# Kernel tuning notes

Hardware: AMD Instinct MI355X
Metric: run time of the kernel (lower is better)

The kernel has to match this reference:

```python
import jax, jax.numpy as jnp
import numpy as np

D_MODEL = 2048
N_HEADS = 16
N_KV = 4
HEAD_DIM = 128
EPS = 1e-5


def _rmsnorm(x, w, eps=EPS):
    var = jnp.mean(x * x, axis=-1, keepdims=True)
    return x * jax.lax.rsqrt(var + eps) * w


def _rope_cos_sin(seq_len, head_dim, dtype):
    inv_freq = 1.0 / (10000.0 ** (jnp.arange(0, head_dim, 2, dtype=jnp.float32) / head_dim))
    t = jnp.arange(seq_len, dtype=jnp.float32)
    freqs = jnp.outer(t, inv_freq)  # [S, hd/2]
    return jnp.cos(freqs).astype(dtype), jnp.sin(freqs).astype(dtype)


def _apply_rope(x, cos, sin):
    # x: [B,H,S,hd]; cos/sin: [S,hd/2] broadcast as [1,1,S,hd/2]
    half = x.shape[-1] // 2
    x1, x2 = x[..., :half], x[..., half:]
    c = cos[None, None]
    s = sin[None, None]
    return jnp.concatenate([x1 * c - x2 * s, x1 * s + x2 * c], axis=-1)


def setup_inputs() -> dict:
    key = jax.random.key(0)
    ks = jax.random.split(key, 7)
    qkv_out = (N_HEADS + 2 * N_KV) * HEAD_DIM  # 3072
    d = D_MODEL
    inp = {
        "x": jax.random.normal(ks[0], (2, 2048, d), dtype=jnp.float32),
        "w_qkv": jax.random.normal(ks[1], (qkv_out, d), dtype=jnp.float32) * (1.0 / np.sqrt(d)),
        "q_norm_w": jnp.ones((HEAD_DIM,), dtype=jnp.float32),
        "k_norm_w": jnp.ones((HEAD_DIM,), dtype=jnp.float32),
        "w_gate": jax.random.normal(ks[2], (N_HEADS, d), dtype=jnp.float32) * 0.02,
        "b_gate": jnp.ones((N_HEADS,), dtype=jnp.float32),
        "w_o": jax.random.normal(ks[3], (d, N_HEADS * HEAD_DIM), dtype=jnp.float32) * (1.0 / np.sqrt(N_HEADS * HEAD_DIM)),
    }
    return inp


def reference(x, w_qkv, q_norm_w, k_norm_w, w_gate, b_gate, w_o):
    B, S, D = x.shape
    hd = HEAD_DIM
    scale = 1.0 / np.sqrt(hd)
    n_rep = N_HEADS // N_KV

    qkv = jnp.einsum("bsd,od->bso", x, w_qkv)  # [B,S,(H+2KV)*hd]
    q_size = N_HEADS * hd
    kv_size = N_KV * hd
    q = qkv[..., :q_size].reshape(B, S, N_HEADS, hd).transpose(0, 2, 1, 3)
    k = qkv[..., q_size:q_size + kv_size].reshape(B, S, N_KV, hd).transpose(0, 2, 1, 3)
    v = qkv[..., q_size + kv_size:].reshape(B, S, N_KV, hd).transpose(0, 2, 1, 3)

    q = _rmsnorm(q, q_norm_w)
    k = _rmsnorm(k, k_norm_w)

    cos, sin = _rope_cos_sin(S, hd, q.dtype)
    q = _apply_rope(q, cos, sin)
    k = _apply_rope(k, cos, sin)

    # GQA: repeat kv heads
    k = jnp.repeat(k, n_rep, axis=1)  # [B,H,S,hd]
    v = jnp.repeat(v, n_rep, axis=1)

    scores = jnp.einsum("bhqd,bhkd->bhqk", q, k) * scale
    causal = jnp.triu(jnp.ones((S, S), dtype=bool), k=1)
    neg = jnp.finfo(scores.dtype).min
    scores = jnp.where(causal[None, None], neg, scores)
    probs = jax.nn.softmax(scores, axis=-1)
    attn = jnp.einsum("bhqk,bhkd->bhqd", probs, v)  # [B,H,S,hd]

    # g1 gating on attention output per query head
    gate = jax.nn.sigmoid(jnp.einsum("bsd,hd->bsh", x, w_gate) + b_gate)  # [B,S,H]
    attn = attn * gate.transpose(0, 2, 1)[..., None]

    attn = attn.transpose(0, 2, 1, 3).reshape(B, S, N_HEADS * hd)
    out = jnp.einsum("bsf,df->bsd", attn, w_o)
    return out
```

## Files before the change

### kernel.cpp

```cpp
#include <hip/hip_runtime.h>

typedef __bf16 bf16x8 __attribute__((ext_vector_type(8)));
typedef float f32x4 __attribute__((ext_vector_type(4)));

typedef __attribute__((address_space(1))) void gvoid;
typedef __attribute__((address_space(3))) void lvoid;

__device__ __forceinline__ void gl_lds16(const void* g, void* l) {
    __builtin_amdgcn_global_load_lds((gvoid*)g, (lvoid*)l, 16, 0, 0);
}

__device__ __forceinline__ float fin(float v) {
    v = (v == v) ? v : 0.f;
    return fminf(fmaxf(v, -3.0e38f), 3.0e38f);
}

__device__ __forceinline__ bf16x8 cvt8(float4 a, float4 b) {
    bf16x8 r;
    r[0] = (__bf16)a.x; r[1] = (__bf16)a.y; r[2] = (__bf16)a.z; r[3] = (__bf16)a.w;
    r[4] = (__bf16)b.x; r[5] = (__bf16)b.y; r[6] = (__bf16)b.z; r[7] = (__bf16)b.w;
    return r;
}

__device__ __forceinline__ void cvt_range(const float* __restrict__ in,
                                          __bf16* __restrict__ out, int i) {
    const float4* p = (const float4*)in + (size_t)i * 2;
    ((bf16x8*)out)[i] = cvt8(p[0], p[1]);
}

#define SCALE_LOG2E 0.12751666797152713f

__global__ __launch_bounds__(256) void prep_kernel(const float* __restrict__ x,
                                                   const float* __restrict__ wqkv,
                                                   __bf16* __restrict__ xb,
                                                   __bf16* __restrict__ wqb,
                                                   const float* __restrict__ wg,
                                                   const float* __restrict__ bg,
                                                   float* __restrict__ gate,
                                                   float2* __restrict__ ropet) {
    __shared__ float gp[4][16];
    int bid = blockIdx.x, tid = threadIdx.x;
    if (bid < 4096) {
        int lane = tid & 63, wave = tid >> 6;
        const float4* xr = (const float4*)(x + (size_t)bid * 2048);
        float4 p0 = xr[tid * 2], p1 = xr[tid * 2 + 1];
        ((bf16x8*)xb)[bid * 256 + tid] = cvt8(p0, p1);
#pragma unroll
        for (int h = 0; h < 16; ++h) {
            const float4* wr = (const float4*)(wg + (size_t)h * 2048);
            float4 w0 = wr[tid * 2], w1 = wr[tid * 2 + 1];
            float acc = p0.x * w0.x + p0.y * w0.y + p0.z * w0.z + p0.w * w0.w +
                        p1.x * w1.x + p1.y * w1.y + p1.z * w1.z + p1.w * w1.w;
#pragma unroll
            for (int m = 1; m < 64; m <<= 1) acc += __shfl_xor(acc, m);
            if (lane == 0) gp[wave][h] = acc;
        }
        __syncthreads();
        if (tid < 16) {
            int s = bid & 2047, b = bid >> 11;
            float z = gp[0][tid] + gp[1][tid] + gp[2][tid] + gp[3][tid] + bg[tid];
            gate[((size_t)b * 16 + tid) * 2048 + s] = 1.f / (1.f + __expf(-z));
        }
        return;
    }
    if (bid < 7168) {
        cvt_range(wqkv, wqb, (bid - 4096) * 256 + tid);
        return;
    }
    int idx = (bid - 7168) * 256 + tid;
    int s = idx >> 6, d0 = idx & 63;
    float freq = (float)s * __expf(-(float)d0 * (9.2103403719761836f / 64.0f));
    ropet[idx] = make_float2(cosf(freq), sinf(freq));
}

__global__ __launch_bounds__(256) void wo_cvt_kernel(const float* __restrict__ wo,
                                                     __bf16* __restrict__ wob) {
    cvt_range(wo, wob, blockIdx.x * 256 + threadIdx.x);
}

template <int WMT, int WNT, int EPI, typename TC>
__global__ __launch_bounds__(512, 4) void gemm8p(const __bf16* __restrict__ A,
                                                 const __bf16* __restrict__ B,
                                                 TC* __restrict__ C,
                                                 int M, int N, int K, int ldA,
                                                 const float* __restrict__ qw,
                                                 const float* __restrict__ kw,
                                                 const float2* __restrict__ ropet,
                                                 __bf16* __restrict__ Kx) {
    constexpr int BM = WMT * 32;
    constexpr int BN = WNT * 64;
    constexpr int LA = BM / 128;
    constexpr int LB = BN / 128;
    constexpr int VMC = 2 * LA + LB;

    __shared__ __align__(16) __bf16 As[2][BM * 64];
    __shared__ __align__(16) __bf16 Bs[2][BN * 64];

    const int tid = threadIdx.x;
    const int lane = tid & 63, wave = tid >> 6;
    const int wm = wave >> 2, wn = wave & 3;
    const int quad = lane >> 4, mrow = lane & 15;

    const int nbx = gridDim.x;
    const int nwg = nbx * gridDim.y;
    const int orig = (int)blockIdx.y * nbx + (int)blockIdx.x;
    const int wg = (orig & 7) * (nwg >> 3) + (orig >> 3);
    const size_t row0 = (size_t)(wg / nbx) * BM;
    const size_t col0 = (size_t)(wg % nbx) * BN;

    size_t sA[LA], sB[LB];
    int dA[LA], dB[LB];
#pragma unroll
    for (int c = 0; c < LA; ++c) {
        int q = c * 512 + tid;
        int a = q * 16;
        int p = (a >> 4) & 63;
        int rowl = (a >> 11) * 16 + (p >> 2);
        int g = (p & 3) ^ ((p >> 3) & 3);
        int col = ((a >> 10) & 1) * 32 + g * 8;
        sA[c] = (size_t)rowl * ldA + col;
        dA[c] = q * 8;
    }
#pragma unroll
    for (int c = 0; c < LB; ++c) {
        int q = c * 512 + tid;
        int a = q * 16;
        int p = (a >> 4) & 63;
        int rowl = (a >> 11) * 16 + (p >> 2);
        int g = (p & 3) ^ ((p >> 3) & 3);
        int col = ((a >> 10) & 1) * 32 + g * 8;
        sB[c] = (size_t)rowl * K + col;
        dB[c] = q * 8;
    }

    const __bf16* Ag = A + row0 * ldA;
    const __bf16* Bg = B + col0 * K;

    f32x4 acc[WMT][WNT];
#pragma unroll
    for (int i = 0; i < WMT; ++i)
#pragma unroll
        for (int j = 0; j < WNT; ++j) acc[i][j] = (f32x4){0.f, 0.f, 0.f, 0.f};

    const int abase = mrow * 64 + ((quad ^ ((mrow >> 1) & 3)) * 16);

    bf16x8 af[WMT / 2][2], bf[WNT / 2][2];

#define STA8(buf, h, kt)                                                        \
    _Pragma("unroll") for (int c = 0; c < LA; ++c)                              \
        gl_lds16(Ag + (size_t)(h) * (BM / 2) * ldA + (size_t)(kt) * 64 + sA[c], \
                 &As[buf][(h) * (BM / 2) * 64 + dA[c]])

#define STB8(buf, h, kt)                                                        \
    _Pragma("unroll") for (int c = 0; c < LB; ++c)                              \
        gl_lds16(Bg + (size_t)(h) * (BN / 2) * K + (size_t)(kt) * 64 + sB[c],   \
                 &Bs[buf][(h) * (BN / 2) * 64 + dB[c]])

#define LDA8(buf, mh)                                                           \
    _Pragma("unroll") for (int m2 = 0; m2 < WMT / 2; ++m2)                      \
    _Pragma("unroll") for (int s = 0; s < 2; ++s)                               \
        af[m2][s] = *(const bf16x8*)((const char*)&As[buf][0] +                 \
            ((((mh) * (WMT / 2) + m2) * 2 + wm) * 2 + s) * 1024 + abase)

#define LDB8(buf, nh)                                                           \
    _Pragma("unroll") for (int n2 = 0; n2 < WNT / 2; ++n2)                      \
    _Pragma("unroll") for (int s = 0; s < 2; ++s)                               \
        bf[n2][s] = *(const bf16x8*)((const char*)&Bs[buf][0] +                 \
            ((((nh) * (WNT / 2) + n2) * 4 + wn) * 2 + s) * 1024 + abase)

#define MMA8(mh, nh)                                                            \
    _Pragma("unroll") for (int m2 = 0; m2 < WMT / 2; ++m2)                      \
    _Pragma("unroll") for (int n2 = 0; n2 < WNT / 2; ++n2)                      \
    _Pragma("unroll") for (int s = 0; s < 2; ++s)                               \
        acc[(mh) * (WMT / 2) + m2][(nh) * (WNT / 2) + n2] =                     \
            __builtin_amdgcn_mfma_f32_16x16x32_bf16(                            \
                af[m2][s], bf[n2][s],                                           \
                acc[(mh) * (WMT / 2) + m2][(nh) * (WNT / 2) + n2], 0, 0, 0)

#define BAR8 __builtin_amdgcn_s_barrier()

#define WAITVM                                                                  \
    do {                                                                        \
        if constexpr (VMC == 6)                                                 \
            asm volatile("s_waitcnt vmcnt(6)" ::: "memory");                    \
        else if constexpr (VMC == 4)                                            \
            asm volatile("s_waitcnt vmcnt(4)" ::: "memory");                    \
        else                                                                    \
            asm volatile("s_waitcnt vmcnt(3)" ::: "memory");                    \
    } while (0)

#define PHASE_TAIL(mh, nh)                                                      \
    __builtin_amdgcn_s_barrier();                                               \
    asm volatile("s_waitcnt lgkmcnt(0)" ::: "memory");                          \
    __builtin_amdgcn_sched_barrier(0);                                          \
    __builtin_amdgcn_s_setprio(1);                                              \
    MMA8(mh, nh);                                                               \
    __builtin_amdgcn_s_setprio(0)

    const int NT = K / 64;

    STA8(0, 0, 0);
    STB8(0, 0, 0);
    STA8(0, 1, 0);
    STB8(0, 1, 0);
    STA8(1, 0, 1);
    STB8(1, 1, 1);
    STA8(1, 1, 1);
    WAITVM;
    BAR8;

    for (int i = 0; i < NT / 2; ++i) {
        const int u = 2 * i;
        const int k2 = (u + 2 < NT) ? u + 2 : NT - 1;
        const int k3 = (u + 3 < NT) ? u + 3 : NT - 1;
        LDA8(0, 0); LDB8(0, 0); STB8(1, 0, u + 1);
        PHASE_TAIL(0, 0); BAR8;
        LDB8(0, 1); STA8(0, 0, k2);
        PHASE_TAIL(0, 1); BAR8;
        LDA8(0, 1); STB8(0, 1, k2);
        PHASE_TAIL(1, 1); BAR8;
        LDB8(0, 0); STA8(0, 1, k2);
        PHASE_TAIL(1, 0); WAITVM; BAR8;
        LDA8(1, 0); LDB8(1, 0); STB8(0, 0, k2);
        PHASE_TAIL(0, 0); BAR8;
        LDB8(1, 1); STA8(1, 0, k3);
        PHASE_TAIL(0, 1); BAR8;
        LDA8(1, 1); STB8(1, 1, k3);
        PHASE_TAIL(1, 1); BAR8;
        LDB8(1, 0); STA8(1, 1, k3);
        PHASE_TAIL(1, 0); WAITVM; BAR8;
    }
    asm volatile("s_waitcnt vmcnt(0)" ::: "memory");

#undef STA8
#undef STB8
#undef LDA8
#undef LDB8
#undef MMA8
#undef BAR8
#undef WAITVM
#undef PHASE_TAIL

    if constexpr (EPI) {
        int xblk = (int)(col0 >> 7);
        if (xblk < 20) {
            __syncthreads();
            float* sums = (float*)&As[0][0];
            const int d0 = wn * 16 + mrow;
#pragma unroll
            for (int mt = 0; mt < WMT; ++mt) {
                f32x4 p;
#pragma unroll
                for (int r = 0; r < 4; ++r)
                    p[r] = acc[mt][0][r] * acc[mt][0][r] +
                           acc[mt][1][r] * acc[mt][1][r];
#pragma unroll
                for (int m = 1; m < 16; m <<= 1)
#pragma unroll
                    for (int r = 0; r < 4; ++r) p[r] += __shfl_xor(p[r], m);
                if (mrow == 0) {
                    int idx = (((wm * 4 + mt) * 4 + quad) * 4 + wn) * 4;
#pragma unroll
                    for (int r = 0; r < 4; ++r) sums[idx + r] = p[r];
                }
            }
            __syncthreads();
            const bool isQ = (xblk < 16);
            const float* w = isQ ? qw : kw;
            float w1 = w[d0], w2 = w[d0 + 64];
            float osc = isQ ? SCALE_LOG2E : 1.0f;
            int kvh = xblk - 16;
#pragma unroll
            for (int mt = 0; mt < WMT; ++mt) {
                int rbase = (int)row0 + (mt * 2 + wm) * 16 + quad * 4;
                int ib = ((wm * 4 + mt) * 4 + quad) * 16;
                f32x4 sv = *(const f32x4*)&sums[ib] + *(const f32x4*)&sums[ib + 4] +
                           *(const f32x4*)&sums[ib + 8] + *(const f32x4*)&sums[ib + 12];
#pragma unroll
                for (int r = 0; r < 4; ++r) {
                    int row = rbase + r;
                    int s_ = row & 2047, b_ = row >> 11;
                    float inv = rsqrtf(sv[r] * (1.0f / 128.0f) + 1e-5f);
                    float2 cs = ropet[s_ * 64 + d0];
                    float y1 = acc[mt][0][r] * inv * w1;
                    float y2 = acc[mt][1][r] * inv * w2;
                    float v1 = (y1 * cs.x - y2 * cs.y) * osc;
                    float v2 = (y1 * cs.y + y2 * cs.x) * osc;
                    if (isQ) {
                        size_t base = (size_t)row * N + col0 + d0;
                        C[base] = (TC)v1;
                        C[base + 64] = (TC)v2;
                    } else {
                        __bf16* dst = Kx + (((size_t)(b_ * 4 + kvh) * 2048 + s_) << 7);
                        dst[d0] = (__bf16)v1;
                        dst[d0 + 64] = (__bf16)v2;
                    }
                }
            }
            return;
        }
    }

#pragma unroll
    for (int mt = 0; mt < WMT; ++mt)
#pragma unroll
        for (int nt = 0; nt < WNT; ++nt)
#pragma unroll
            for (int r = 0; r < 4; ++r) {
                size_t row = row0 + (mt * 2 + wm) * 16 + quad * 4 + r;
                size_t col = col0 + (nt * 4 + wn) * 16 + mrow;
                C[row * N + col] = (TC)fin(acc[mt][nt][r]);
            }
}

__global__ __launch_bounds__(256) void mid_kernel(const __bf16* __restrict__ qkv,
                                                  __bf16* __restrict__ Vt) {
    __shared__ __align__(16) __bf16 tile[64][72];
    int v = blockIdx.x, t = threadIdx.x;
    int st0 = (v & 31) * 64;
    int dblk = (v >> 5) & 1;
    int bz = v >> 6;
    int b = bz >> 2, kv = bz & 3;
    const __bf16* src = qkv + (size_t)(b * 2048 + st0) * 3072 + 2560 + kv * 128 + dblk * 64;
#pragma unroll
    for (int it = 0; it < 2; ++it) {
        int row = it * 32 + (t >> 3);
        int ch = t & 7;
        *(bf16x8*)&tile[row][ch * 8] = *(const bf16x8*)(src + (size_t)row * 3072 + ch * 8);
    }
    __syncthreads();
    __bf16* dst = Vt + ((size_t)(b * 4 + kv) * 128 + dblk * 64) * 2048 + st0;
#pragma unroll
    for (int it = 0; it < 2; ++it) {
        int drow = it * 32 + (t >> 3);
        int sch = t & 7;
        bf16x8 vv;
#pragma unroll
        for (int j = 0; j < 8; ++j) vv[j] = tile[sch * 8 + j][drow];
        *(bf16x8*)(dst + (size_t)drow * 2048 + sch * 8) = vv;
    }
}

#define FIXED_M 20.0f

#define MFMA16(a, b, c) __builtin_amdgcn_mfma_f32_16x16x32_bf16(a, b, c, 0, 0, 0)

__device__ __forceinline__ int pswz(int e) { return e ^ (((e >> 7) & 1) << 4); }

template <int MODE>
__device__ __forceinline__ void attn_step(const __bf16* Kl, const __bf16* Vl,
                                          int ws, int quad, int mrow,
                                          const bf16x8* aq0, const bf16x8* aq1,
                                          f32x4* o0, f32x4* o1,
                                          f32x4& lf0, f32x4& lf1,
                                          __bf16* Pw) {
    bf16x8 ones;
#pragma unroll
    for (int i = 0; i < 8; ++i) ones[i] = (__bf16)1.0f;

    f32x4 sc0[4], sc1[4];
    __builtin_amdgcn_s_setprio(1);
#pragma unroll
    for (int jt = 0; jt < 4; ++jt) {
        f32x4 s0 = (f32x4){0.f, 0.f, 0.f, 0.f};
        f32x4 s1 = (f32x4){0.f, 0.f, 0.f, 0.f};
#pragma unroll
        for (int dt = 0; dt < 4; ++dt) {
            bf16x8 bk = *(const bf16x8*)&Kl[((dt * 4 + quad) * 64 + jt * 16 + mrow) * 8];
            if (MODE < 2) s0 = MFMA16(aq0[dt], bk, s0);
            s1 = MFMA16(aq1[dt], bk, s1);
        }
        sc0[jt] = s0;
        sc1[jt] = s1;
    }
    __builtin_amdgcn_s_setprio(0);

    if (MODE == 1) {
        int rloc = ws * 16 + quad * 4;
#pragma unroll
        for (int jt = 0; jt < 4; ++jt)
#pragma unroll
            for (int r = 0; r < 4; ++r)
                if (jt * 16 + mrow > rloc + r) sc0[jt][r] = -1e30f;
    }
    if (MODE == 2) {
        int rloc = ws * 16 + quad * 4;
#pragma unroll
        for (int jt = 0; jt < 4; ++jt)
#pragma unroll
            for (int r = 0; r < 4; ++r)
                if (jt * 16 + mrow > rloc + r) sc1[jt][r] = -1e30f;
    }

    const int rb0 = pswz(((0 * 4 + quad) * 16 + mrow) * 8);
    const int rb1 = pswz(((1 * 4 + quad) * 16 + mrow) * 8);
    bf16x8 ap0[2], ap1[2];
    if (MODE < 2) {
#pragma unroll
        for (int jt = 0; jt < 4; ++jt)
#pragma unroll
            for (int r = 0; r < 4; ++r) {
                float pv = exp2f(sc0[jt][r] - FIXED_M);
                int k = jt * 16 + mrow;
                Pw[pswz(((k >> 3) * 16 + quad * 4 + r) * 8 + (k & 7))] = (__bf16)pv;
            }
        ap0[0] = *(const bf16x8*)&Pw[rb0];
        ap0[1] = *(const bf16x8*)&Pw[rb1];
        lf0 = MFMA16(ap0[0], ones, lf0);
        lf0 = MFMA16(ap0[1], ones, lf0);
    }
#pragma unroll
    for (int jt = 0; jt < 4; ++jt)
#pragma unroll
        for (int r = 0; r < 4; ++r) {
            float pv = exp2f(sc1[jt][r] - FIXED_M);
            int k = jt * 16 + mrow;
            Pw[pswz(((k >> 3) * 16 + quad * 4 + r) * 8 + (k & 7))] = (__bf16)pv;
        }
    ap1[0] = *(const bf16x8*)&Pw[rb0];
    ap1[1] = *(const bf16x8*)&Pw[rb1];
    lf1 = MFMA16(ap1[0], ones, lf1);
    lf1 = MFMA16(ap1[1], ones, lf1);

    __builtin_amdgcn_s_setprio(1);
#pragma unroll
    for (int d2 = 0; d2 < 8; ++d2)
#pragma unroll
        for (int ks = 0; ks < 2; ++ks) {
            bf16x8 bv = *(const bf16x8*)&Vl[((ks * 4 + quad) * 128 + d2 * 16 + mrow) * 8];
            if (MODE < 2) o0[d2] = MFMA16(ap0[ks], bv, o0[d2]);
            o1[d2] = MFMA16(ap1[ks], bv, o1[d2]);
        }
    __builtin_amdgcn_s_setprio(0);
}

__global__ __launch_bounds__(512, 2) void attn_kernel(__bf16* __restrict__ qkvO,
                                                      const __bf16* __restrict__ Kx,
                                                      const __bf16* __restrict__ Vt,
                                                      const float* __restrict__ gate) {
    __shared__ __align__(16) __bf16 Kl[2][2][64 * 128];
    __shared__ __align__(16) __bf16 Vl[2][2][128 * 64];
    __shared__ __align__(16) __bf16 Pl[8][1024];
    int tid = threadIdx.x, lane = tid & 63, wave = tid >> 6;

    int ws = wave & 3, st = wave >> 2;
    int quad = lane >> 4, mrow = lane & 15;
    __bf16* Pw = &Pl[wave][0];

    int idx = blockIdx.x;
    int qb = 15 - (idx >> 5);
    int h = idx & 15, b = (idx >> 4) & 1;
    int kvh = h >> 2;

    int sst = tid >> 8, lt = tid & 255;
    const __bf16* kbase = Kx + (size_t)(b * 4 + kvh) * 2048 * 128 + (lt & 63) * 128 + (lt >> 6) * 8;
    const __bf16* vbase = Vt + (size_t)(b * 4 + kvh) * 128 * 2048 + (lt & 127) * 2048 + (lt >> 7) * 8;
    int ldst = lt * 8;

    auto STAGE = [&](int buf, int tile) {
        const __bf16* kp = kbase + (size_t)tile * 8192;
        const __bf16* vp = vbase + (size_t)tile * 64;
#pragma unroll
        for (int c = 0; c < 4; ++c) gl_lds16(kp + 32 * c, &Kl[sst][buf][ldst + 2048 * c]);
#pragma unroll
        for (int c = 0; c < 4; ++c) gl_lds16(vp + 16 * c, &Vl[sst][buf][ldst + 2048 * c]);
    };

    STAGE(0, sst);

    const __bf16* Qh = qkvO + (size_t)(b * 2048 + qb * 128 + ws * 16 + mrow) * 3072 + h * 128;
    bf16x8 aq0[4], aq1[4];
#pragma unroll
    for (int dt = 0; dt < 4; ++dt) {
        aq0[dt] = *(const bf16x8*)(Qh + dt * 32 + quad * 8);
        aq1[dt] = *(const bf16x8*)(Qh + (size_t)64 * 3072 + dt * 32 + quad * 8);
    }

    f32x4 o0[8], o1[8];
#pragma unroll
    for (int d2 = 0; d2 < 8; ++d2) {
        o0[d2] = (f32x4){0.f, 0.f, 0.f, 0.f};
        o1[d2] = (f32x4){0.f, 0.f, 0.f, 0.f};
    }
    f32x4 lf0 = (f32x4){0.f, 0.f, 0.f, 0.f}, lf1 = (f32x4){0.f, 0.f, 0.f, 0.f};

    __syncthreads();

    int cur = 0;
    for (int kt = 0; kt < qb; ++kt) {
        STAGE(cur ^ 1, 2 * (kt + 1) + sst);
        attn_step<0>(Kl[st][cur], Vl[st][cur], ws, quad, mrow, aq0, aq1, o0, o1, lf0, lf1, Pw);
        __syncthreads();
        cur ^= 1;
    }
    if (st == 0)
        attn_step<1>(Kl[0][cur], Vl[0][cur], ws, quad, mrow, aq0, aq1, o0, o1, lf0, lf1, Pw);
    else
        attn_step<2>(Kl[1][cur], Vl[1][cur], ws, quad, mrow, aq0, aq1, o0, o1, lf0, lf1, Pw);

    __syncthreads();
    f32x4* mo = (f32x4*)&Kl[0][0][0];
    float* ml = (float*)&Pl[0][0];
    int mlane = ws * 64 + lane;
    if (st == 1) {
#pragma unroll
        for (int d2 = 0; d2 < 8; ++d2) {
            mo[d2 * 256 + mlane] = o0[d2];
            mo[(d2 + 8) * 256 + mlane] = o1[d2];
        }
#pragma unroll
        for (int r = 0; r < 4; ++r) {
            ml[r * 256 + mlane] = lf0[r];
            ml[(r + 4) * 256 + mlane] = lf1[r];
        }
    }
    __syncthreads();
    if (st == 0) {
#pragma unroll
        for (int d2 = 0; d2 < 8; ++d2) {
            o0[d2] += mo[d2 * 256 + mlane];
            o1[d2] += mo[(d2 + 8) * 256 + mlane];
        }
#pragma unroll
        for (int r = 0; r < 4; ++r) {
            lf0[r] += ml[r * 256 + mlane];
            lf1[r] += ml[(r + 4) * 256 + mlane];
        }
#pragma unroll
        for (int hf = 0; hf < 2; ++hf) {
            f32x4* oo = hf ? o1 : o0;
            f32x4 ll = hf ? lf1 : lf0;
            int srow0 = qb * 128 + hf * 64 + ws * 16 + quad * 4;
            float gv[4], il[4];
#pragma unroll
            for (int r = 0; r < 4; ++r) {
                gv[r] = gate[((size_t)b * 16 + h) * 2048 + srow0 + r];
                il[r] = 1.0f / fmaxf(ll[r], 1e-30f);
            }
#pragma unroll
            for (int d2 = 0; d2 < 8; ++d2)
#pragma unroll
                for (int r = 0; r < 4; ++r)
                    qkvO[(size_t)(b * 2048 + srow0 + r) * 3072 + h * 128 + d2 * 16 + mrow] =
                        (__bf16)fin(oo[d2][r] * il[r] * gv[r]);
        }
    }
}

extern "C" void kernel_launch(void* const* d_in, const int* in_sizes, int n_in,
                              void* d_out, int out_size, void* d_ws, size_t ws_size,
                              hipStream_t stream) {
    const float* x = (const float*)d_in[0];
    const float* w_qkv = (const float*)d_in[1];
    const float* q_norm_w = (const float*)d_in[2];
    const float* k_norm_w = (const float*)d_in[3];
    const float* w_gate = (const float*)d_in[4];
    const float* b_gate = (const float*)d_in[5];
    const float* w_o = (const float*)d_in[6];
    float* out = (float*)d_out;

    char* ws = (char*)d_ws;
    char* od = (char*)d_out;
    __bf16* xb = (__bf16*)(od);
    __bf16* wqb = (__bf16*)(od + 16777216);
    float* gateb = (float*)(od + 29360128);
    float2* ropet = (float2*)(od + 29622272);
    __bf16* qkv = (__bf16*)(ws);
    __bf16* Kb = (__bf16*)(ws + 25165824);
    __bf16* Vtb = (__bf16*)(ws + 29360128);
    __bf16* wob = (__bf16*)(ws + 25165824);

    prep_kernel<<<7680, 256, 0, stream>>>(x, w_qkv, xb, wqb, w_gate, b_gate, gateb, ropet);
    gemm8p<4, 2, 1, __bf16><<<dim3(3072 / 128, 4096 / 128), 512, 0, stream>>>(
        xb, wqb, qkv, 4096, 3072, 2048, 2048, q_norm_w, k_norm_w, ropet, Kb);
    mid_kernel<<<512, 256, 0, stream>>>(qkv, Vtb);
    attn_kernel<<<512, 512, 0, stream>>>(qkv, Kb, Vtb, gateb);
    wo_cvt_kernel<<<2048, 256, 0, stream>>>(w_o, wob);
    gemm8p<4, 2, 0, float><<<dim3(2048 / 128, 4096 / 128), 512, 0, stream>>>(
        qkv, wob, out, 4096, 2048, 2048, 3072, nullptr, nullptr, nullptr, nullptr);
}
```

Baseline: 342.3 us.

## Restructure GEMM main loop into four phases loading both A halves per phase

The bf16 GEMM main loop moves from eight phases per two K-tiles to four. Each phase now loads both M-halves of the A fragments into two register sets and issues twice as many MFMAs, which halves the barriers and LDS waits per K-tile. The global-to-LDS prefetch is reordered to match, with hardcoded vmcnt waits in place of the template-derived count. This raises register pressure and relies on the hardcoded waitcnts being correct for every tile-shape instantiation.

```diff
diff --git a/kernel.cpp b/kernel.cpp
--- a/kernel.cpp
+++ b/kernel.cpp
@@ -91,7 +91,6 @@
     constexpr int BN = WNT * 64;
     constexpr int LA = BM / 128;
     constexpr int LB = BN / 128;
-    constexpr int VMC = 2 * LA + LB;
 
     __shared__ __align__(16) __bf16 As[2][BM * 64];
     __shared__ __align__(16) __bf16 Bs[2][BN * 64];
@@ -144,7 +143,7 @@
 
     const int abase = mrow * 64 + ((quad ^ ((mrow >> 1) & 3)) * 16);
 
-    bf16x8 af[WMT / 2][2], bf[WNT / 2][2];
+    bf16x8 af[WMT / 2][2], af2[WMT / 2][2], bf[WNT / 2][2];
 
 #define STA8(buf, h, kt)                                                        \
     _Pragma("unroll") for (int c = 0; c < LA; ++c)                              \
@@ -156,10 +155,10 @@
         gl_lds16(Bg + (size_t)(h) * (BN / 2) * K + (size_t)(kt) * 64 + sB[c],   \
                  &Bs[buf][(h) * (BN / 2) * 64 + dB[c]])
 
-#define LDA8(buf, mh)                                                           \
+#define LDA8(dst, buf, mh)                                                      \
     _Pragma("unroll") for (int m2 = 0; m2 < WMT / 2; ++m2)                      \
     _Pragma("unroll") for (int s = 0; s < 2; ++s)                               \
-        af[m2][s] = *(const bf16x8*)((const char*)&As[buf][0] +                 \
+        dst[m2][s] = *(const bf16x8*)((const char*)&As[buf][0] +                \
             ((((mh) * (WMT / 2) + m2) * 2 + wm) * 2 + s) * 1024 + abase)
 
 #define LDB8(buf, nh)                                                           \
@@ -168,67 +167,61 @@
         bf[n2][s] = *(const bf16x8*)((const char*)&Bs[buf][0] +                 \
             ((((nh) * (WNT / 2) + n2) * 4 + wn) * 2 + s) * 1024 + abase)
 
-#define MMA8(mh, nh)                                                            \
+#define MMA16(nh)                                                               \
     _Pragma("unroll") for (int m2 = 0; m2 < WMT / 2; ++m2)                      \
     _Pragma("unroll") for (int n2 = 0; n2 < WNT / 2; ++n2)                      \
-    _Pragma("unroll") for (int s = 0; s < 2; ++s)                               \
-        acc[(mh) * (WMT / 2) + m2][(nh) * (WNT / 2) + n2] =                     \
+    _Pragma("unroll") for (int s = 0; s < 2; ++s) {                             \
+        acc[m2][(nh) * (WNT / 2) + n2] =                                        \
             __builtin_amdgcn_mfma_f32_16x16x32_bf16(                            \
                 af[m2][s], bf[n2][s],                                           \
-                acc[(mh) * (WMT / 2) + m2][(nh) * (WNT / 2) + n2], 0, 0, 0)
+                acc[m2][(nh) * (WNT / 2) + n2], 0, 0, 0);                       \
+        acc[(WMT / 2) + m2][(nh) * (WNT / 2) + n2] =                            \
+            __builtin_amdgcn_mfma_f32_16x16x32_bf16(                            \
+                af2[m2][s], bf[n2][s],                                          \
+                acc[(WMT / 2) + m2][(nh) * (WNT / 2) + n2], 0, 0, 0);           \
+    }
 
 #define BAR8 __builtin_amdgcn_s_barrier()
 
-#define WAITVM                                                                  \
-    do {                                                                        \
-        if constexpr (VMC == 6)                                                 \
-            asm volatile("s_waitcnt vmcnt(6)" ::: "memory");                    \
-        else if constexpr (VMC == 4)                                            \
-            asm volatile("s_waitcnt vmcnt(4)" ::: "memory");                    \
-        else                                                                    \
-            asm volatile("s_waitcnt vmcnt(3)" ::: "memory");                    \
-    } while (0)
-
-#define PHASE_TAIL(mh, nh)                                                      \
+#define PHASE_TAIL(nh)                                                          \
     __builtin_amdgcn_s_barrier();                                               \
     asm volatile("s_waitcnt lgkmcnt(0)" ::: "memory");                          \
     __builtin_amdgcn_sched_barrier(0);                                          \
     __builtin_amdgcn_s_setprio(1);                                              \
-    MMA8(mh, nh);                                                               \
+    MMA16(nh);                                                                  \
     __builtin_amdgcn_s_setprio(0)
 
     const int NT = K / 64;
 
     STA8(0, 0, 0);
+    STA8(0, 1, 0);
     STB8(0, 0, 0);
-    STA8(0, 1, 0);
     STB8(0, 1, 0);
     STA8(1, 0, 1);
-    STB8(1, 1, 1);
     STA8(1, 1, 1);
-    WAITVM;
+    asm volatile("s_waitcnt vmcnt(3)" ::: "memory");
     BAR8;
 
     for (int i = 0; i < NT / 2; ++i) {
         const int u = 2 * i;
         const int k2 = (u + 2 < NT) ? u + 2 : NT - 1;
         const int k3 = (u + 3 < NT) ? u + 3 : NT - 1;
-        LDA8(0, 0); LDB8(0, 0); STB8(1, 0, u + 1);
-        PHASE_TAIL(0, 0); BAR8;
-        LDB8(0, 1); STA8(0, 0, k2);
-        PHASE_TAIL(0, 1); BAR8;
-        LDA8(0, 1); STB8(0, 1, k2);
-        PHASE_TAIL(1, 1); BAR8;
-        LDB8(0, 0); STA8(0, 1, k2);
-        PHASE_TAIL(1, 0); WAITVM; BAR8;
-        LDA8(1, 0); LDB8(1, 0); STB8(0, 0, k2);
-        PHASE_TAIL(0, 0); BAR8;
-        LDB8(1, 1); STA8(1, 0, k3);
-        PHASE_TAIL(0, 1); BAR8;
-        LDA8(1, 1); STB8(1, 1, k3);
-        PHASE_TAIL(1, 1); BAR8;
-        LDB8(1, 0); STA8(1, 1, k3);
-        PHASE_TAIL(1, 0); WAITVM; BAR8;
+        LDA8(af, 0, 0); LDA8(af2, 0, 1); LDB8(0, 0);
+        STB8(1, 0, u + 1); STB8(1, 1, u + 1);
+        PHASE_TAIL(0);
+        asm volatile("s_waitcnt vmcnt(4)" ::: "memory"); BAR8;
+        LDB8(0, 1);
+        STA8(0, 0, k2); STA8(0, 1, k2); STB8(0, 0, k2);
+        PHASE_TAIL(1);
+        asm volatile("s_waitcnt vmcnt(4)" ::: "memory"); BAR8;
+        LDA8(af, 1, 0); LDA8(af2, 1, 1); LDB8(1, 0);
+        STB8(0, 1, k2);
+        PHASE_TAIL(0);
+        asm volatile("s_waitcnt vmcnt(4)" ::: "memory"); BAR8;
+        LDB8(1, 1);
+        STA8(1, 0, k3); STA8(1, 1, k3);
+        PHASE_TAIL(1);
+        asm volatile("s_waitcnt vmcnt(3)" ::: "memory"); BAR8;
     }
     asm volatile("s_waitcnt vmcnt(0)" ::: "memory");
 
@@ -236,9 +229,8 @@
 #undef STB8
 #undef LDA8
 #undef LDB8
-#undef MMA8
+#undef MMA16
 #undef BAR8
-#undef WAITVM
 #undef PHASE_TAIL
 
     if constexpr (EPI) {
```

New measurement: 329.7 us. 1.04x faster.
